# Kernel tuning notes

Hardware: AMD Instinct MI355X
Metric: run time of the kernel (lower is better)

Reference implementation:

```python
import jax, jax.numpy as jnp
import numpy as np

N = 50000
E = 800000
IN_C = 128
HID = 32
HEADS = 4
OUT_C = 128
NEG_SLOPE = 0.2


def setup_inputs() -> dict:
    key = jax.random.key(0)
    ks = jax.random.split(key, 12)
    x = jax.random.normal(ks[0], (N, IN_C), dtype=jnp.float32)
    edge_index = jax.random.randint(ks[1], (2, E), 0, N, dtype=jnp.int32)
    s1 = 1.0 / np.sqrt(IN_C)
    s2 = 1.0 / np.sqrt(HEADS * HID)
    return {
        "x": x,
        "edge_index": edge_index,
        # conv1: in_channels -> hidden*heads, concat=True
        "W1l": jax.random.normal(ks[2], (IN_C, HEADS * HID), dtype=jnp.float32) * s1,
        "W1r": jax.random.normal(ks[3], (IN_C, HEADS * HID), dtype=jnp.float32) * s1,
        "att1": jax.random.normal(ks[4], (HEADS, HID), dtype=jnp.float32) * (1.0 / np.sqrt(HID)),
        "b1": jnp.zeros((HEADS * HID,), dtype=jnp.float32),
        # conv2: hidden*heads -> out_channels, heads=1, concat=False
        "W2l": jax.random.normal(ks[5], (HEADS * HID, OUT_C), dtype=jnp.float32) * s2,
        "W2r": jax.random.normal(ks[6], (HEADS * HID, OUT_C), dtype=jnp.float32) * s2,
        "att2": jax.random.normal(ks[7], (1, OUT_C), dtype=jnp.float32) * (1.0 / np.sqrt(OUT_C)),
        "b2": jnp.zeros((OUT_C,), dtype=jnp.float32),
    }


def gatv2_conv(x, src, dst, Wl, Wr, att, bias, heads, out_per_head, concat):
    n = x.shape[0]
    xl = (x @ Wl).reshape(n, heads, out_per_head)   # source transform [N,H,C]
    xr = (x @ Wr).reshape(n, heads, out_per_head)   # target transform [N,H,C]
    m = xl[src] + xr[dst]                           # [E,H,C]
    e = jnp.sum(jax.nn.leaky_relu(m, NEG_SLOPE) * att, axis=-1)  # [E,H]
    # segment softmax over incoming edges of each destination node
    mx = jax.ops.segment_max(e, dst, num_segments=n)             # [N,H]
    ex = jnp.exp(e - mx[dst])                                    # [E,H]
    denom = jax.ops.segment_sum(ex, dst, num_segments=n)         # [N,H]
    alpha = ex / jnp.where(denom[dst] == 0, 1.0, denom[dst])     # [E,H]
    out = jax.ops.segment_sum(alpha[:, :, None] * xl[src], dst, num_segments=n)  # [N,H,C]
    if concat:
        out = out.reshape(n, heads * out_per_head)
    else:
        out = out.mean(axis=1)
    return out + bias


def reference(x, edge_index, W1l, W1r, att1, b1, W2l, W2r, att2, b2):
    src, dst = edge_index[0], edge_index[1]
    h = gatv2_conv(x, src, dst, W1l, W1r, att1, b1, HEADS, HID, concat=True)
    h = jax.nn.elu(h)
    out = gatv2_conv(h, src, dst, W2l, W2r, att2, b2, 1, OUT_C, concat=False)
    return out
```

## Files before the change

kernel.cpp:

```cpp
#include <hip/hip_runtime.h>
#include <math.h>

#define IN_C 128
#define NEG_SLOPE 0.2f
#define LOG2E 1.44269504f

typedef unsigned int uint_t;
typedef unsigned short ushort_t;
typedef _Float16 half8_t __attribute__((ext_vector_type(8)));
typedef _Float16 half2_t __attribute__((ext_vector_type(2)));
typedef float floatx4 __attribute__((ext_vector_type(4)));

__device__ __forceinline__ float fdot2f(half2_t a, half2_t b, float c) {
#if __has_builtin(__builtin_amdgcn_fdot2)
    return __builtin_amdgcn_fdot2(a, b, c, false);
#else
    return fmaf((float)a[1], (float)b[1], fmaf((float)a[0], (float)b[0], c));
#endif
}
#define H2(v, i) ((half2_t){(v)[2 * (i)], (v)[2 * (i) + 1]})

__device__ __forceinline__ float fexp2(float x) {
#if __has_builtin(__builtin_amdgcn_exp2f)
    return __builtin_amdgcn_exp2f(x);
#else
    return exp2f(x);
#endif
}

template <int CTRL>
__device__ __forceinline__ float dpp_addf(float x) {
    int y = __builtin_amdgcn_update_dpp(0, __float_as_int(x), CTRL, 0xF, 0xF, true);
    return x + __int_as_float(y);
}

#define XPAD 136
template <bool IN_HALF>
__global__ __launch_bounds__(256) void transform_mfma(
        const void* __restrict__ xin,
        const float* __restrict__ Wl,
        const float* __restrict__ Wr,
        _Float16* __restrict__ outl,
        _Float16* __restrict__ outr, int n) {
    __shared__ _Float16 xs[16 * XPAD + 8];
    const int tid  = threadIdx.x;
    const int wv   = tid >> 6;
    const int l    = tid & 63;
    const int lm   = l & 15;
    const int quad = l >> 4;
    const int kb   = quad * 8;

    const float* Wsel = (wv < 2) ? Wl : Wr;
    _Float16*    osel = (wv < 2) ? outl : outr;
    const int nbase = (wv & 1) * 64;
    half8_t bw[4][4];
#pragma unroll
    for (int t = 0; t < 4; ++t) {
        const int ncol = nbase + t * 16 + lm;
#pragma unroll
        for (int K = 0; K < 4; ++K) {
            const int k0 = K * 32 + kb;
            half8_t h;
#pragma unroll
            for (int j = 0; j < 8; ++j)
                h[j] = (_Float16)Wsel[(size_t)(k0 + j) * IN_C + ncol];
            bw[t][K] = h;
        }
    }

    const int nStrips = (n + 15) >> 4;
    for (int s = blockIdx.x; s < nStrips; s += gridDim.x) {
        const int row0 = s * 16;
        __syncthreads();
        {
            const int srow = tid >> 4;
            const int scol = (tid & 15) * 8;
            const int grow = row0 + srow;
            half8_t h;
#pragma unroll
            for (int j = 0; j < 8; ++j) h[j] = (_Float16)0.f;
            if (grow < n) {
                if constexpr (IN_HALF) {
                    h = *(const half8_t*)&((const _Float16*)xin)[(size_t)grow * IN_C + scol];
                } else {
                    const float4 v0 = *(const float4*)&((const float*)xin)[(size_t)grow * IN_C + scol];
                    const float4 v1 = *(const float4*)&((const float*)xin)[(size_t)grow * IN_C + scol + 4];
                    h[0] = (_Float16)v0.x; h[1] = (_Float16)v0.y;
                    h[2] = (_Float16)v0.z; h[3] = (_Float16)v0.w;
                    h[4] = (_Float16)v1.x; h[5] = (_Float16)v1.y;
                    h[6] = (_Float16)v1.z; h[7] = (_Float16)v1.w;
                }
            }
            *(half8_t*)&xs[srow * XPAD + scol] = h;
        }
        __syncthreads();
        half8_t af[4];
#pragma unroll
        for (int K = 0; K < 4; ++K)
            af[K] = *(half8_t*)&xs[lm * XPAD + K * 32 + kb];
        floatx4 acc[4];
#pragma unroll
        for (int t = 0; t < 4; ++t) acc[t] = (floatx4){0.f, 0.f, 0.f, 0.f};
#pragma unroll
        for (int t = 0; t < 4; ++t)
#pragma unroll
            for (int K = 0; K < 4; ++K)
                acc[t] = __builtin_amdgcn_mfma_f32_16x16x32_f16(af[K], bw[t][K], acc[t], 0, 0, 0);
#pragma unroll
        for (int t = 0; t < 4; ++t) {
            const int col = nbase + t * 16 + lm;
#pragma unroll
            for (int r = 0; r < 4; ++r) {
                const int row = row0 + quad * 4 + r;
                if (row < n) osel[(size_t)row * IN_C + col] = (_Float16)acc[t][r];
            }
        }
    }
}

__global__ void hist_kernel(const int* __restrict__ dst, int* __restrict__ cnt, int E) {
    int e = blockIdx.x * blockDim.x + threadIdx.x;
    if (e < E) atomicAdd(&cnt[dst[e]], 1);
}

__global__ void scan_block_sums(const int* __restrict__ cnt, int* __restrict__ part, int n) {
    __shared__ int sdata[256];
    int t = threadIdx.x;
    int i = blockIdx.x * 256 + t;
    sdata[t] = (i < n) ? ((cnt[i] + 3) & ~3) : 0;
    __syncthreads();
    for (int o = 128; o >= 1; o >>= 1) {
        if (t < o) sdata[t] += sdata[t + o];
        __syncthreads();
    }
    if (t == 0) part[blockIdx.x] = sdata[0];
}

__global__ void scan_part_excl(int* __restrict__ part, int nb) {
    __shared__ int buf[1024];
    int t = threadIdx.x;
    int v = (t < nb) ? part[t] : 0;
    buf[t] = v;
    __syncthreads();
    for (int o = 1; o < 1024; o <<= 1) {
        int a = (t >= o) ? buf[t - o] : 0;
        __syncthreads();
        buf[t] += a;
        __syncthreads();
    }
    if (t < nb) part[t] = buf[t] - v;
}

__global__ void scan_final(const int* __restrict__ cnt, const int* __restrict__ part,
                           int* __restrict__ rowptr, int* __restrict__ cursor, int n) {
    __shared__ int buf[256];
    int t = threadIdx.x;
    int i = blockIdx.x * 256 + t;
    int v = (i < n) ? ((cnt[i] + 3) & ~3) : 0;
    buf[t] = v;
    __syncthreads();
    for (int o = 1; o < 256; o <<= 1) {
        int a = (t >= o) ? buf[t - o] : 0;
        __syncthreads();
        buf[t] += a;
        __syncthreads();
    }
    int excl = part[blockIdx.x] + buf[t] - v;
    if (i < n) { rowptr[i] = excl; cursor[i] = excl; }
    if (i == n - 1) rowptr[n] = excl + v;
}

__global__ void scatter_csr(const int* __restrict__ src,
                            const int* __restrict__ dst,
                            int* __restrict__ cursor,
                            ushort_t* __restrict__ gsrc, int E) {
    int e = blockIdx.x * blockDim.x + threadIdx.x;
    if (e >= E) return;
    int pos = atomicAdd(&cursor[dst[e]], 1);
    gsrc[pos] = (ushort_t)src[e];
}

template <int LAYER>
__global__ __launch_bounds__(256) void node_fused(
        const _Float16* __restrict__ xlb,
        const _Float16* __restrict__ xr,
        const float* __restrict__ att,
        const int* __restrict__ rowptr,
        const int* __restrict__ cnt,
        const ushort_t* __restrict__ gsrc,
        const float* __restrict__ bias,
        void* __restrict__ outp, int N) {
    const int l = threadIdx.x & 63;
    const int q = l & 15;
    const int d = blockIdx.x * 16 + (threadIdx.x >> 4);
    if (d >= N) return;
    const int beg = rowptr[d];
    const int deg = cnt[d];
    const int nt  = (deg + 3) >> 2;
    const int cb  = q * 8;

    const half8_t xrv = *(const half8_t*)&xr[(size_t)d * IN_C + cb];
    const float4 A0 = *(const float4*)&att[cb];
    const float4 A1 = *(const float4*)&att[cb + 4];
    const float afv[8] = {A0.x, A0.y, A0.z, A0.w, A1.x, A1.y, A1.z, A1.w};
    half8_t a6, a4;
#pragma unroll
    for (int j = 0; j < 8; ++j) {
        a6[j] = (_Float16)(0.6f * LOG2E * afv[j]);
        a4[j] = (_Float16)(0.4f * LOG2E * afv[j]);
    }

    float m = -1e30f, ls = 0.f;
    float acc[8] = {0.f, 0.f, 0.f, 0.f, 0.f, 0.f, 0.f, 0.f};

    const uint2* gp = (const uint2*)(gsrc + beg);
    uint2 gcur;
    half8_t xc[4];
    if (nt > 0) {
        gcur = gp[0];
        uint_t i0 = gcur.x & 0xffffu, i1 = gcur.x >> 16;
        uint_t i2 = gcur.y & 0xffffu, i3 = gcur.y >> 16;
        xc[0] = *(const half8_t*)(xlb + (i0 << 7) + cb);
        xc[1] = *(const half8_t*)(xlb + (i1 << 7) + cb);
        xc[2] = *(const half8_t*)(xlb + (i2 << 7) + cb);
        xc[3] = *(const half8_t*)(xlb + (i3 << 7) + cb);
    }

    for (int t = 0; t < nt; ++t) {
        const int tn = (t + 1 < nt) ? t + 1 : t;
        uint2 gnext = gp[tn];
        float f[4];
#pragma unroll
        for (int u = 0; u < 4; ++u) {
            half8_t tv = xc[u] + xrv;
            uint4 tu = __builtin_bit_cast(uint4, tv);
            tu.x &= 0x7fff7fffu; tu.y &= 0x7fff7fffu;
            tu.z &= 0x7fff7fffu; tu.w &= 0x7fff7fffu;
            half8_t av = __builtin_bit_cast(half8_t, tu);
            float p = 0.f;
#pragma unroll
            for (int j = 0; j < 4; ++j) p = fdot2f(H2(tv, j), H2(a6, j), p);
#pragma unroll
            for (int j = 0; j < 4; ++j) p = fdot2f(H2(av, j), H2(a4, j), p);
            p = dpp_addf<0xB1>(p);
            p = dpp_addf<0x4E>(p);
            if (LAYER == 2) {
                p = dpp_addf<0x141>(p);
                p = dpp_addf<0x140>(p);
            }
            f[u] = (4 * t + u < deg) ? p : -1e30f;
        }
        float bm = fmaxf(fmaxf(f[0], f[1]), fmaxf(f[2], f[3]));
        if (!__all(bm <= m + 5.7708f)) {
            float nm = fmaxf(m, bm);
            float fc = fexp2(m - nm);
            ls *= fc;
#pragma unroll
            for (int j = 0; j < 8; ++j) acc[j] *= fc;
            m = nm;
        }
        half8_t xn[4];
        {
            uint_t i0 = gnext.x & 0xffffu, i1 = gnext.x >> 16;
            uint_t i2 = gnext.y & 0xffffu, i3 = gnext.y >> 16;
            xn[0] = *(const half8_t*)(xlb + (i0 << 7) + cb);
            xn[1] = *(const half8_t*)(xlb + (i1 << 7) + cb);
            xn[2] = *(const half8_t*)(xlb + (i2 << 7) + cb);
            xn[3] = *(const half8_t*)(xlb + (i3 << 7) + cb);
        }
#pragma unroll
        for (int u = 0; u < 4; ++u) {
            float wgt = fexp2(f[u] - m);
            ls += wgt;
#pragma unroll
            for (int j = 0; j < 8; ++j)
                acc[j] = fmaf((float)xc[u][j], wgt, acc[j]);
        }
#pragma unroll
        for (int u = 0; u < 4; ++u) xc[u] = xn[u];
        gcur = gnext;
    }

    const float inv = (ls > 0.f) ? 1.f / ls : 0.f;
    const float4 b0 = *(const float4*)&bias[cb];
    const float4 b1 = *(const float4*)&bias[cb + 4];
    const float bf[8] = {b0.x, b0.y, b0.z, b0.w, b1.x, b1.y, b1.z, b1.w};
    if (LAYER == 1) {
        half8_t h;
#pragma unroll
        for (int j = 0; j < 8; ++j) {
            float o = acc[j] * inv + bf[j];
            o = (o > 0.f) ? o : fexp2(o * LOG2E) - 1.f;
            h[j] = (_Float16)o;
        }
        *(half8_t*)&((_Float16*)outp)[(size_t)d * IN_C + cb] = h;
    } else {
        float4 o1, o2;
        o1.x = acc[0] * inv + bf[0]; o1.y = acc[1] * inv + bf[1];
        o1.z = acc[2] * inv + bf[2]; o1.w = acc[3] * inv + bf[3];
        o2.x = acc[4] * inv + bf[4]; o2.y = acc[5] * inv + bf[5];
        o2.z = acc[6] * inv + bf[6]; o2.w = acc[7] * inv + bf[7];
        *(float4*)&((float*)outp)[(size_t)d * IN_C + cb]     = o1;
        *(float4*)&((float*)outp)[(size_t)d * IN_C + cb + 4] = o2;
    }
}

extern "C" void kernel_launch(void* const* d_in, const int* in_sizes, int n_in,
                              void* d_out, int out_size, void* d_ws, size_t ws_size,
                              hipStream_t stream) {
    const float* x    = (const float*)d_in[0];
    const int*   ei   = (const int*)d_in[1];
    const float* W1l  = (const float*)d_in[2];
    const float* W1r  = (const float*)d_in[3];
    const float* att1 = (const float*)d_in[4];
    const float* b1   = (const float*)d_in[5];
    const float* W2l  = (const float*)d_in[6];
    const float* W2r  = (const float*)d_in[7];
    const float* att2 = (const float*)d_in[8];
    const float* b2   = (const float*)d_in[9];

    const int N = in_sizes[0] / IN_C;
    const int E = in_sizes[1] / 2;
    const int* src = ei;
    const int* dst = ei + E;

    float* ws = (float*)d_ws;
    size_t o = 0;
    _Float16* xlh = (_Float16*)(ws + o); o += (size_t)N * IN_C / 2;
    _Float16* xrh = (_Float16*)(ws + o); o += (size_t)N * IN_C / 2;
    _Float16* hb  = (_Float16*)(ws + o); o += (size_t)N * IN_C / 2;
    int* iws    = (int*)(ws + o);
    int* rowptr = iws;
    int* cnt    = iws + (N + 1);
    int* cursor = iws + (N + 1) + N;
    int* part   = iws + (N + 1) + 2 * N;
    ushort_t* gsrc = (ushort_t*)(iws + (N + 1) + 2 * N + 1024);
    const size_t gsrc_bytes = ((size_t)E + 4 * (size_t)N + 64) * sizeof(ushort_t);

    hipMemsetAsync(cnt, 0, (size_t)N * 4, stream);
    hipMemsetAsync(gsrc, 0, gsrc_bytes, stream);

    const int B = 256;
    const int nb = (N + 255) / 256;
    hist_kernel<<<(E + B - 1) / B, B, 0, stream>>>(dst, cnt, E);
    scan_block_sums<<<nb, 256, 0, stream>>>(cnt, part, N);
    scan_part_excl<<<1, 1024, 0, stream>>>(part, nb);
    scan_final<<<nb, 256, 0, stream>>>(cnt, part, rowptr, cursor, N);
    scatter_csr<<<(E + B - 1) / B, B, 0, stream>>>(src, dst, cursor, gsrc, E);

    transform_mfma<false><<<512, 256, 0, stream>>>(x, W1l, W1r, xlh, xrh, N);
    node_fused<1><<<(N + 15) / 16, 256, 0, stream>>>(xlh, xrh, att1, rowptr, cnt, gsrc, b1, hb, N);

    transform_mfma<true><<<512, 256, 0, stream>>>(hb, W2l, W2r, xlh, xrh, N);
    node_fused<2><<<(N + 15) / 16, 256, 0, stream>>>(xlh, xrh, att2, rowptr, cnt, gsrc, b2, d_out, N);
}
```

Baseline: 283.3 us.

## Fuse layer-1 transform with histogram and process nodes in degree-sorted order

Merges the first dense transform and the in-degree histogram into one launch, with separate block ranges for MFMA work and atomics. Adds a 64-bin bucketing of nodes by padded degree (counted in scan_final, prefix-summed in the scatter kernel, scattered by a new kernel) so node_fused threads in a wavefront handle nodes of similar degree. The aim is less loop divergence across the 16-lane groups and fewer launches, paid for with an extra kernel, more atomics and an indirect order lookup that scatters output writes.

```diff
diff --git a/kernel.cpp b/kernel.cpp
--- a/kernel.cpp
+++ b/kernel.cpp
@@ -4,6 +4,8 @@
 #define IN_C 128
 #define NEG_SLOPE 0.2f
 #define LOG2E 1.44269504f
+#define TFB 512
+#define HB  1024
 
 typedef unsigned int uint_t;
 typedef unsigned short ushort_t;
@@ -36,12 +38,12 @@
 
 #define XPAD 136
 template <bool IN_HALF>
-__global__ __launch_bounds__(256) void transform_mfma(
+__device__ __forceinline__ void tf_body(
         const void* __restrict__ xin,
         const float* __restrict__ Wl,
         const float* __restrict__ Wr,
         _Float16* __restrict__ outl,
-        _Float16* __restrict__ outr, int n) {
+        _Float16* __restrict__ outr, int n, int bid, int nBlocks) {
     __shared__ _Float16 xs[16 * XPAD + 8];
     const int tid  = threadIdx.x;
     const int wv   = tid >> 6;
@@ -69,7 +71,7 @@
     }
 
     const int nStrips = (n + 15) >> 4;
-    for (int s = blockIdx.x; s < nStrips; s += gridDim.x) {
+    for (int s = bid; s < nStrips; s += nBlocks) {
         const int row0 = s * 16;
         __syncthreads();
         {
@@ -118,9 +120,29 @@
     }
 }
 
-__global__ void hist_kernel(const int* __restrict__ dst, int* __restrict__ cnt, int E) {
-    int e = blockIdx.x * blockDim.x + threadIdx.x;
-    if (e < E) atomicAdd(&cnt[dst[e]], 1);
+__global__ __launch_bounds__(256) void tf1_hist(
+        const float* __restrict__ x,
+        const float* __restrict__ Wl,
+        const float* __restrict__ Wr,
+        _Float16* __restrict__ outl,
+        _Float16* __restrict__ outr, int n,
+        const int* __restrict__ dst, int* __restrict__ cnt, int E) {
+    if (blockIdx.x < TFB) {
+        tf_body<false>(x, Wl, Wr, outl, outr, n, blockIdx.x, TFB);
+    } else {
+        const int stride = HB * 256;
+        for (int e = (blockIdx.x - TFB) * 256 + threadIdx.x; e < E; e += stride)
+            atomicAdd(&cnt[dst[e]], 1);
+    }
+}
+
+__global__ __launch_bounds__(256) void transform_mfma_h(
+        const _Float16* __restrict__ xin,
+        const float* __restrict__ Wl,
+        const float* __restrict__ Wr,
+        _Float16* __restrict__ outl,
+        _Float16* __restrict__ outr, int n) {
+    tf_body<true>(xin, Wl, Wr, outl, outr, n, blockIdx.x, gridDim.x);
 }
 
 __global__ void scan_block_sums(const int* __restrict__ cnt, int* __restrict__ part, int n) {
@@ -152,7 +174,8 @@
 }
 
 __global__ void scan_final(const int* __restrict__ cnt, const int* __restrict__ part,
-                           int* __restrict__ rowptr, int* __restrict__ cursor, int n) {
+                           int* __restrict__ rowptr, int* __restrict__ cursor,
+                           int* __restrict__ bcnt, int n) {
     __shared__ int buf[256];
     int t = threadIdx.x;
     int i = blockIdx.x * 256 + t;
@@ -166,18 +189,39 @@
         __syncthreads();
     }
     int excl = part[blockIdx.x] + buf[t] - v;
-    if (i < n) { rowptr[i] = excl; cursor[i] = excl; }
+    if (i < n) {
+        rowptr[i] = excl; cursor[i] = excl;
+        atomicAdd(&bcnt[min(v >> 2, 63)], 1);
+    }
     if (i == n - 1) rowptr[n] = excl + v;
 }
 
-__global__ void scatter_csr(const int* __restrict__ src,
-                            const int* __restrict__ dst,
-                            int* __restrict__ cursor,
-                            ushort_t* __restrict__ gsrc, int E) {
-    int e = blockIdx.x * blockDim.x + threadIdx.x;
+__global__ void scatter_bscan(const int* __restrict__ src,
+                              const int* __restrict__ dst,
+                              int* __restrict__ cursor,
+                              ushort_t* __restrict__ gsrc, int E,
+                              const int* __restrict__ bcnt, int* __restrict__ bcur) {
+    if (blockIdx.x == 0) {
+        if (threadIdx.x == 0) {
+            int s = 0;
+#pragma unroll
+            for (int i = 0; i < 64; ++i) { bcur[i] = s; s += bcnt[i]; }
+        }
+        return;
+    }
+    int e = (blockIdx.x - 1) * blockDim.x + threadIdx.x;
     if (e >= E) return;
     int pos = atomicAdd(&cursor[dst[e]], 1);
     gsrc[pos] = (ushort_t)src[e];
+}
+
+__global__ void bucket_scatter(const int* __restrict__ cnt, int* __restrict__ bcur,
+                               int* __restrict__ order, int N) {
+    int d = blockIdx.x * blockDim.x + threadIdx.x;
+    if (d >= N) return;
+    int bin = min((cnt[d] + 3) >> 2, 63);
+    int pos = atomicAdd(&bcur[bin], 1);
+    order[pos] = d;
 }
 
 template <int LAYER>
@@ -188,12 +232,14 @@
         const int* __restrict__ rowptr,
         const int* __restrict__ cnt,
         const ushort_t* __restrict__ gsrc,
+        const int* __restrict__ order,
         const float* __restrict__ bias,
         void* __restrict__ outp, int N) {
     const int l = threadIdx.x & 63;
     const int q = l & 15;
-    const int d = blockIdx.x * 16 + (threadIdx.x >> 4);
-    if (d >= N) return;
+    const int ds = blockIdx.x * 16 + (threadIdx.x >> 4);
+    if (ds >= N) return;
+    const int d = order[ds];
     const int beg = rowptr[d];
     const int deg = cnt[d];
     const int nt  = (deg + 3) >> 2;
@@ -214,12 +260,11 @@
     float acc[8] = {0.f, 0.f, 0.f, 0.f, 0.f, 0.f, 0.f, 0.f};
 
     const uint2* gp = (const uint2*)(gsrc + beg);
-    uint2 gcur;
     half8_t xc[4];
     if (nt > 0) {
-        gcur = gp[0];
-        uint_t i0 = gcur.x & 0xffffu, i1 = gcur.x >> 16;
-        uint_t i2 = gcur.y & 0xffffu, i3 = gcur.y >> 16;
+        uint2 g0 = gp[0];
+        uint_t i0 = g0.x & 0xffffu, i1 = g0.x >> 16;
+        uint_t i2 = g0.y & 0xffffu, i3 = g0.y >> 16;
         xc[0] = *(const half8_t*)(xlb + (i0 << 7) + cb);
         xc[1] = *(const half8_t*)(xlb + (i1 << 7) + cb);
         xc[2] = *(const half8_t*)(xlb + (i2 << 7) + cb);
@@ -278,7 +323,6 @@
         }
 #pragma unroll
         for (int u = 0; u < 4; ++u) xc[u] = xn[u];
-        gcur = gnext;
     }
 
     const float inv = (ls > 0.f) ? 1.f / ls : 0.f;
@@ -331,26 +375,29 @@
     _Float16* hb  = (_Float16*)(ws + o); o += (size_t)N * IN_C / 2;
     int* iws    = (int*)(ws + o);
     int* rowptr = iws;
-    int* cnt    = iws + (N + 1);
-    int* cursor = iws + (N + 1) + N;
-    int* part   = iws + (N + 1) + 2 * N;
-    ushort_t* gsrc = (ushort_t*)(iws + (N + 1) + 2 * N + 1024);
+    int* cnt    = rowptr + (N + 1);
+    int* bcnt   = cnt + N;
+    int* bcur   = bcnt + 64;
+    int* cursor = bcur + 64;
+    int* part   = cursor + N;
+    int* order  = part + 1024;
+    ushort_t* gsrc = (ushort_t*)(order + N);
     const size_t gsrc_bytes = ((size_t)E + 4 * (size_t)N + 64) * sizeof(ushort_t);
 
-    hipMemsetAsync(cnt, 0, (size_t)N * 4, stream);
+    hipMemsetAsync(cnt, 0, ((size_t)N + 64) * 4, stream);
     hipMemsetAsync(gsrc, 0, gsrc_bytes, stream);
 
     const int B = 256;
     const int nb = (N + 255) / 256;
-    hist_kernel<<<(E + B - 1) / B, B, 0, stream>>>(dst, cnt, E);
+    tf1_hist<<<TFB + HB, 256, 0, stream>>>(x, W1l, W1r, xlh, xrh, N, dst, cnt, E);
     scan_block_sums<<<nb, 256, 0, stream>>>(cnt, part, N);
     scan_part_excl<<<1, 1024, 0, stream>>>(part, nb);
-    scan_final<<<nb, 256, 0, stream>>>(cnt, part, rowptr, cursor, N);
-    scatter_csr<<<(E + B - 1) / B, B, 0, stream>>>(src, dst, cursor, gsrc, E);
-
-    transform_mfma<false><<<512, 256, 0, stream>>>(x, W1l, W1r, xlh, xrh, N);
-    node_fused<1><<<(N + 15) / 16, 256, 0, stream>>>(xlh, xrh, att1, rowptr, cnt, gsrc, b1, hb, N);
-
-    transform_mfma<true><<<512, 256, 0, stream>>>(hb, W2l, W2r, xlh, xrh, N);
-    node_fused<2><<<(N + 15) / 16, 256, 0, stream>>>(xlh, xrh, att2, rowptr, cnt, gsrc, b2, d_out, N);
-}
+    scan_final<<<nb, 256, 0, stream>>>(cnt, part, rowptr, cursor, bcnt, N);
+    scatter_bscan<<<1 + (E + B - 1) / B, B, 0, stream>>>(src, dst, cursor, gsrc, E, bcnt, bcur);
+    bucket_scatter<<<nb, 256, 0, stream>>>(cnt, bcur, order, N);
+
+    node_fused<1><<<(N + 15) / 16, 256, 0, stream>>>(xlh, xrh, att1, rowptr, cnt, gsrc, order, b1, hb, N);
+
+    transform_mfma_h<<<512, 256, 0, stream>>>(hb, W2l, W2r, xlh, xrh, N);
+    node_fused<2><<<(N + 15) / 16, 256, 0, stream>>>(xlh, xrh, att2, rowptr, cnt, gsrc, order, b2, d_out, N);
+}
```

Result: slower. 847.3 us (+199.1%).
